# Kernel tuning notes

Hardware: AMD Instinct MI355X
Metric: run time of the kernel (lower is better)

The kernel has to match this reference:

```python
import jax, jax.numpy as jnp
import numpy as np

WS = 11
SIGMA = 1.5
CH = 3
C1 = (0.01 * 255.0) ** 2  # 6.5025
C2 = (0.03 * 255.0) ** 2  # 58.5225


def _gauss_window():
    # 1D Gaussian -> outer product -> depthwise kernel [C, 1, ws, ws] (OIHW)
    coords = jnp.arange(WS, dtype=jnp.float32) - WS // 2
    g = jnp.exp(-coords ** 2 / (2.0 * SIGMA ** 2))
    g = g / g.sum()
    w2d = g[:, None] * g[None, :]
    return jnp.tile(w2d[None, None], (CH, 1, 1, 1))


def _dwconv(x, win):
    pad = WS // 2
    return jax.lax.conv_general_dilated(
        x, win, window_strides=(1, 1), padding=[(pad, pad), (pad, pad)],
        feature_group_count=CH,
        dimension_numbers=('NCHW', 'OIHW', 'NCHW'))


def setup_inputs() -> dict:
    key = jax.random.key(0)
    k1, k2 = jax.random.split(key)
    shape = (32, 3, 512, 512)
    img_gen = jax.random.uniform(k1, shape, jnp.float32, -1.0, 1.0)
    img_ref = jax.random.uniform(k2, shape, jnp.float32, -1.0, 1.0)
    return {"img_gen": img_gen, "img_ref": img_ref}


def reference(img_gen, img_ref):
    gen = (img_gen + 1.0) * 0.5
    ref = (img_ref + 1.0) * 0.5
    win = _gauss_window()

    mu1 = _dwconv(gen, win)
    mu2 = _dwconv(ref, win)
    mu1_sq = mu1 * mu1
    mu2_sq = mu2 * mu2
    mu1_mu2 = mu1 * mu2
    sigma1_sq = _dwconv(gen * gen, win) - mu1_sq
    sigma2_sq = _dwconv(ref * ref, win) - mu2_sq
    sigma12 = _dwconv(gen * ref, win) - mu1_mu2

    ssim_map = ((2.0 * mu1_mu2 + C1) * (2.0 * sigma12 + C2)) / (
        (mu1_sq + mu2_sq + C1) * (sigma1_sq + sigma2_sq + C2))
    return 1.0 - ssim_map.mean()
```

## Files before the change

kernel.cpp:

```cpp
#include <hip/hip_runtime.h>

typedef float v2f __attribute__((ext_vector_type(2)));

#define TX 64
#define TY 8
#define MY 8
#define BYR (TY * MY)
#define WIN 26
#define HSTR 65
#define IMW 512
#define IMH 512
#define NPLANES 96
#define NBX (IMW / TX)
#define NBY (IMH / BYR)
#define NBLOCKS (NBX * NBY * NPLANES)

#define GW0 0.00102838f
#define GW1 0.00759877f
#define GW2 0.03600077f
#define GW3 0.10936069f
#define GW4 0.21300553f
#define GW5 0.26601172f

__device__ __forceinline__ void pkfma(v2f& acc, v2f a, v2f b) {
  asm("v_pk_fma_f32 %0, %1, %2, %0" : "+v"(acc) : "v"(a), "v"(b));
}
__device__ __forceinline__ v2f pkmul(v2f a, v2f b) {
  v2f d;
  asm("v_pk_mul_f32 %0, %1, %2" : "=v"(d) : "v"(a), "v"(b));
  return d;
}

__device__ __forceinline__ void hblur4(
    const float* __restrict__ gp, const float* __restrict__ rp,
    float* __restrict__ sq, int x0, bool fast, int nrows, int gy0,
    int slot0, int tid) {
  if (tid >= nrows * 16) return;
  const float GW[11] = {GW0, GW1, GW2, GW3, GW4, GW5,
                        GW4, GW3, GW2, GW1, GW0};
  const int r = tid >> 4;
  const int xs = (tid & 15) * 4;
  const int gy = gy0 + r;
  int slot = slot0 + r;
  if (slot >= WIN) slot -= WIN;
  const int xbase = x0 + xs - 8;
  const float* grow = gp + (size_t)gy * IMW;
  const float* rrow = rp + (size_t)gy * IMW;

  v2f P[14];
#define PUT1(idx, gc, rc)                                                    \
  do {                                                                       \
    if ((idx) >= 3 && (idx) <= 16)                                           \
      P[(idx) - 3] = (v2f){fmaf(0.5f, (gc), 0.5f), fmaf(0.5f, (rc), 0.5f)};  \
  } while (0)
  if (fast) {
#pragma unroll
    for (int k = 0; k < 5; ++k) {
      const float4 g4 = *(const float4*)(grow + xbase + 4 * k);
      const float4 r4 = *(const float4*)(rrow + xbase + 4 * k);
      PUT1(4 * k + 0, g4.x, r4.x);
      PUT1(4 * k + 1, g4.y, r4.y);
      PUT1(4 * k + 2, g4.z, r4.z);
      PUT1(4 * k + 3, g4.w, r4.w);
    }
  } else {
    const bool rowok = (gy >= 0) & (gy < IMH);
#pragma unroll
    for (int k = 0; k < 5; ++k) {
      const int c = xbase + 4 * k;
      const bool ok = rowok && (c >= 0) && (c < IMW);
      float4 g4 = make_float4(-1.f, -1.f, -1.f, -1.f);
      float4 r4 = g4;
      if (ok) {
        g4 = *(const float4*)(grow + c);
        r4 = *(const float4*)(rrow + c);
      }
      PUT1(4 * k + 0, g4.x, r4.x);
      PUT1(4 * k + 1, g4.y, r4.y);
      PUT1(4 * k + 2, g4.z, r4.z);
      PUT1(4 * k + 3, g4.w, r4.w);
    }
  }
#undef PUT1

  v2f accP[4], accQ[4];
  float accS[4];
#pragma unroll
  for (int o = 0; o < 4; ++o) {
    accP[o] = (v2f){0.f, 0.f};
    accQ[o] = (v2f){0.f, 0.f};
    accS[o] = 0.f;
  }

#pragma unroll
  for (int p = 0; p < 14; ++p) {
    const v2f pv = P[p];
    const v2f qv = pkmul(pv, pv);
    const float sv = pv.x * pv.y;
    const int olo = (p - 10 < 0) ? 0 : p - 10;
    const int ohi = (p < 3) ? p : 3;
#pragma unroll
    for (int o = olo; o <= ohi; ++o) {
      const float wt = GW[p - o];
      const v2f wv = (v2f){wt, wt};
      pkfma(accP[o], wv, pv);
      pkfma(accQ[o], wv, qv);
      accS[o] = fmaf(wt, sv, accS[o]);
    }
  }

  float* dst = sq + slot * (5 * HSTR) + xs;
#pragma unroll
  for (int o = 0; o < 4; ++o) dst[0 * HSTR + o] = accP[o].x;
#pragma unroll
  for (int o = 0; o < 4; ++o) dst[1 * HSTR + o] = accP[o].y;
#pragma unroll
  for (int o = 0; o < 4; ++o) dst[2 * HSTR + o] = accQ[o].x;
#pragma unroll
  for (int o = 0; o < 4; ++o) dst[3 * HSTR + o] = accQ[o].y;
#pragma unroll
  for (int o = 0; o < 4; ++o) dst[4 * HSTR + o] = accS[o];
}

__device__ __forceinline__ float ssim_px(v2f mu, v2f ee, float e12) {
  const float C1 = 6.5025f, C2 = 58.5225f;
  const float mu1 = mu.x, mu2 = mu.y, e1 = ee.x, e2 = ee.y;
  const float m12 = mu1 * mu2;
  const float m1s = mu1 * mu1;
  const float m2s = mu2 * mu2;
  const float num = (2.f * m12 + C1) * (2.f * (e12 - m12) + C2);
  const float den = (m1s + m2s + C1) * ((e1 - m1s) + (e2 - m2s) + C2);
  return __fdividef(num, den);
}

__device__ __forceinline__ float phase2(
    const float* __restrict__ sq, int wb, int col, int r0) {
  const float GW[11] = {GW0, GW1, GW2, GW3, GW4, GW5,
                        GW4, GW3, GW2, GW1, GW0};
  v2f mu[4], ee[4];
  float e12[4];
#pragma unroll
  for (int o = 0; o < 4; ++o) {
    mu[o] = (v2f){0.f, 0.f};
    ee[o] = (v2f){0.f, 0.f};
    e12[o] = 0.f;
  }
#pragma unroll
  for (int i = 0; i < 15; ++i) {
    int slot = wb + r0 + i;
    if (slot >= WIN) slot -= WIN;
    const float* rowp = sq + slot * (5 * HSTR) + col;
    const v2f hp = (v2f){rowp[0 * HSTR], rowp[1 * HSTR]};
    const v2f hq = (v2f){rowp[2 * HSTR], rowp[3 * HSTR]};
    const float hsv = rowp[4 * HSTR];
    const int olo = (i - 10 < 0) ? 0 : i - 10;
    const int ohi = (i < 3) ? i : 3;
#pragma unroll
    for (int o = olo; o <= ohi; ++o) {
      const float wt = GW[i - o];
      const v2f wv = (v2f){wt, wt};
      pkfma(mu[o], wv, hp);
      pkfma(ee[o], wv, hq);
      e12[o] = fmaf(wt, hsv, e12[o]);
    }
  }
  return (ssim_px(mu[0], ee[0], e12[0]) + ssim_px(mu[1], ee[1], e12[1])) +
         (ssim_px(mu[2], ee[2], e12[2]) + ssim_px(mu[3], ee[3], e12[3]));
}

__global__ __launch_bounds__(256, 4) void ssim_main(
    const float* __restrict__ gen, const float* __restrict__ ref,
    double* __restrict__ partial) {
  __shared__ float s_q[WIN][5][HSTR];
  float* const sq = &s_q[0][0][0];

  const int tid = threadIdx.x;
  const int bid = blockIdx.x;
  const int bx = bid & (NBX - 1);
  const int rem = bid >> 3;
  const int by = rem & (NBY - 1);
  const int plane = rem >> 3;
  const int x0 = bx * TX;
  const int Y0 = by * BYR;
  const float* gp = gen + (size_t)plane * (IMW * IMH);
  const float* rp = ref + (size_t)plane * (IMW * IMH);
  const bool ix = (bx >= 1) & (bx <= NBX - 2);

  const int col = tid & 63;
  const int r0 = __builtin_amdgcn_readfirstlane((tid >> 6 >= 3) ? 4 : 0);

  hblur4(gp, rp, sq, x0, ix & (by > 0), 16, Y0 - 5, 0, tid);
  hblur4(gp, rp, sq, x0, ix, 2, Y0 + 11, 16, tid);
  __syncthreads();

  double acc = 0.0;
  int wbase = 0;
  int sbase = 18;
#pragma unroll 1
  for (int c = 0; c < MY; ++c) {
    if (tid < 128) {
      if (c < MY - 1) {
        const int gy0 = Y0 + 13 + TY * c;
        hblur4(gp, rp, sq, x0, ix && (gy0 + TY <= IMH), TY, gy0, sbase, tid);
      }
    } else {
      acc += (double)phase2(sq, wbase, col, r0);
    }
    __syncthreads();
    wbase += TY;
    if (wbase >= WIN) wbase -= WIN;
    sbase += TY;
    if (sbase >= WIN) sbase -= WIN;
  }

#pragma unroll
  for (int off = 32; off > 0; off >>= 1) acc += __shfl_down(acc, off, 64);
  double* swsum = (double*)sq;
  if ((tid & 63) == 0) swsum[tid >> 6] = acc;
  __syncthreads();
  if (tid == 0) partial[bid] = swsum[0] + swsum[1] + swsum[2] + swsum[3];
}

__global__ void ssim_reduce(const double* __restrict__ partial,
                            float* __restrict__ out) {
  const int tid = threadIdx.x;
  double s = 0.0;
  for (int i = tid; i < NBLOCKS; i += 256) s += partial[i];
#pragma unroll
  for (int off = 32; off > 0; off >>= 1) s += __shfl_down(s, off, 64);
  __shared__ double sd[4];
  if ((tid & 63) == 0) sd[tid >> 6] = s;
  __syncthreads();
  if (tid == 0) {
    const double npix = (double)NPLANES * (double)IMW * (double)IMH;
    out[0] = (float)(1.0 - (sd[0] + sd[1] + sd[2] + sd[3]) / npix);
  }
}

extern "C" void kernel_launch(void* const* d_in, const int* in_sizes, int n_in,
                              void* d_out, int out_size, void* d_ws, size_t ws_size,
                              hipStream_t stream) {
  (void)in_sizes; (void)n_in; (void)out_size; (void)ws_size;
  const float* gen = (const float*)d_in[0];
  const float* ref = (const float*)d_in[1];
  double* partial = (double*)d_ws;
  ssim_main<<<NBLOCKS, 256, 0, stream>>>(gen, ref, partial);
  ssim_reduce<<<1, 256, 0, stream>>>(partial, (float*)d_out);
}
```

Measured before the change: 325.8 us.

## Make each wavefront own a 32-column strip with a private ring buffer, dropping block barriers

Restructures the SSIM kernel so each 64-lane wavefront processes its own 32-wide, 256-row strip. Each wave keeps a private 18-row shared-memory ring of horizontal blur results and alternates vertical-blur and horizontal-blur steps itself, so the per-chunk __syncthreads calls go away. Partial sums are written per wave, and the launch-bounds occupancy hint drops from 4 to 3 blocks. In exchange, the narrower strips recompute more horizontal halo columns per output, each wave runs a serial chain of 32 chunks, and the compute/load split between waves inside a block is lost.

```diff
diff --git a/kernel.cpp b/kernel.cpp
--- a/kernel.cpp
+++ b/kernel.cpp
@@ -2,18 +2,19 @@
 
 typedef float v2f __attribute__((ext_vector_type(2)));
 
-#define TX 64
 #define TY 8
-#define MY 8
-#define BYR (TY * MY)
-#define WIN 26
-#define HSTR 65
+#define WIN 18
+#define CST 33
+#define RST (5 * CST)
+#define SWV (WIN * RST)
 #define IMW 512
 #define IMH 512
 #define NPLANES 96
-#define NBX (IMW / TX)
-#define NBY (IMH / BYR)
-#define NBLOCKS (NBX * NBY * NPLANES)
+#define NSX 16
+#define NSEG 2
+#define NCH 32
+#define NWAVES (NSX * NSEG * NPLANES)
+#define NBLOCKS (NWAVES / 4)
 
 #define GW0 0.00102838f
 #define GW1 0.00759877f
@@ -31,17 +32,15 @@
   return d;
 }
 
-__device__ __forceinline__ void hblur4(
+__device__ __forceinline__ void hblur(
     const float* __restrict__ gp, const float* __restrict__ rp,
     float* __restrict__ sq, int x0, bool fast, int nrows, int gy0,
-    int slot0, int tid) {
-  if (tid >= nrows * 16) return;
+    int slot0, int hr, int xs) {
+  if (hr >= nrows) return;
   const float GW[11] = {GW0, GW1, GW2, GW3, GW4, GW5,
                         GW4, GW3, GW2, GW1, GW0};
-  const int r = tid >> 4;
-  const int xs = (tid & 15) * 4;
-  const int gy = gy0 + r;
-  int slot = slot0 + r;
+  const int gy = gy0 + hr;
+  int slot = slot0 + hr;
   if (slot >= WIN) slot -= WIN;
   const int xbase = x0 + xs - 8;
   const float* grow = gp + (size_t)gy * IMW;
@@ -109,17 +108,17 @@
     }
   }
 
-  float* dst = sq + slot * (5 * HSTR) + xs;
-#pragma unroll
-  for (int o = 0; o < 4; ++o) dst[0 * HSTR + o] = accP[o].x;
-#pragma unroll
-  for (int o = 0; o < 4; ++o) dst[1 * HSTR + o] = accP[o].y;
-#pragma unroll
-  for (int o = 0; o < 4; ++o) dst[2 * HSTR + o] = accQ[o].x;
-#pragma unroll
-  for (int o = 0; o < 4; ++o) dst[3 * HSTR + o] = accQ[o].y;
-#pragma unroll
-  for (int o = 0; o < 4; ++o) dst[4 * HSTR + o] = accS[o];
+  float* dst = sq + slot * RST + xs;
+#pragma unroll
+  for (int o = 0; o < 4; ++o) dst[0 * CST + o] = accP[o].x;
+#pragma unroll
+  for (int o = 0; o < 4; ++o) dst[1 * CST + o] = accP[o].y;
+#pragma unroll
+  for (int o = 0; o < 4; ++o) dst[2 * CST + o] = accQ[o].x;
+#pragma unroll
+  for (int o = 0; o < 4; ++o) dst[3 * CST + o] = accQ[o].y;
+#pragma unroll
+  for (int o = 0; o < 4; ++o) dst[4 * CST + o] = accS[o];
 }
 
 __device__ __forceinline__ float ssim_px(v2f mu, v2f ee, float e12) {
@@ -133,7 +132,7 @@
   return __fdividef(num, den);
 }
 
-__device__ __forceinline__ float phase2(
+__device__ __forceinline__ float vchunk(
     const float* __restrict__ sq, int wb, int col, int r0) {
   const float GW[11] = {GW0, GW1, GW2, GW3, GW4, GW5,
                         GW4, GW3, GW2, GW1, GW0};
@@ -146,13 +145,13 @@
     e12[o] = 0.f;
   }
 #pragma unroll
-  for (int i = 0; i < 15; ++i) {
+  for (int i = 0; i < 14; ++i) {
     int slot = wb + r0 + i;
     if (slot >= WIN) slot -= WIN;
-    const float* rowp = sq + slot * (5 * HSTR) + col;
-    const v2f hp = (v2f){rowp[0 * HSTR], rowp[1 * HSTR]};
-    const v2f hq = (v2f){rowp[2 * HSTR], rowp[3 * HSTR]};
-    const float hsv = rowp[4 * HSTR];
+    const float* rowp = sq + slot * RST + col;
+    const v2f hp = (v2f){rowp[0 * CST], rowp[1 * CST]};
+    const v2f hq = (v2f){rowp[2 * CST], rowp[3 * CST]};
+    const float hsv = rowp[4 * CST];
     const int olo = (i - 10 < 0) ? 0 : i - 10;
     const int ohi = (i < 3) ? i : 3;
 #pragma unroll
@@ -168,64 +167,58 @@
          (ssim_px(mu[2], ee[2], e12[2]) + ssim_px(mu[3], ee[3], e12[3]));
 }
 
-__global__ __launch_bounds__(256, 4) void ssim_main(
+__global__ __launch_bounds__(256, 3) void ssim_main(
     const float* __restrict__ gen, const float* __restrict__ ref,
     double* __restrict__ partial) {
-  __shared__ float s_q[WIN][5][HSTR];
-  float* const sq = &s_q[0][0][0];
+  __shared__ float ring[4][SWV];
 
   const int tid = threadIdx.x;
-  const int bid = blockIdx.x;
-  const int bx = bid & (NBX - 1);
-  const int rem = bid >> 3;
-  const int by = rem & (NBY - 1);
-  const int plane = rem >> 3;
-  const int x0 = bx * TX;
-  const int Y0 = by * BYR;
+  const int wv = tid >> 6;
+  const int lane = tid & 63;
+  const int wid = (blockIdx.x << 2) | wv;
+  const int plane = wid >> 5;
+  const int rem = wid & 31;
+  const int sx = rem & 15;
+  const int seg = rem >> 4;
+  const int x0 = sx * 32;
+  const int Y0 = seg * 256;
   const float* gp = gen + (size_t)plane * (IMW * IMH);
   const float* rp = ref + (size_t)plane * (IMW * IMH);
-  const bool ix = (bx >= 1) & (bx <= NBX - 2);
-
-  const int col = tid & 63;
-  const int r0 = __builtin_amdgcn_readfirstlane((tid >> 6 >= 3) ? 4 : 0);
-
-  hblur4(gp, rp, sq, x0, ix & (by > 0), 16, Y0 - 5, 0, tid);
-  hblur4(gp, rp, sq, x0, ix, 2, Y0 + 11, 16, tid);
-  __syncthreads();
+  float* const sq = &ring[wv][0];
+  const bool fx = (sx >= 1) & (sx <= NSX - 2);
+
+  const int hr = lane >> 3;
+  const int xs = (lane & 7) * 4;
+  const int col = lane & 31;
+  const int r0 = (lane >> 5) * 4;
+
+  hblur(gp, rp, sq, x0, fx & (seg > 0), 8, Y0 - 5, 0, hr, xs);
+  hblur(gp, rp, sq, x0, fx, 8, Y0 + 3, 8, hr, xs);
+  hblur(gp, rp, sq, x0, fx, 2, Y0 + 11, 16, hr, xs);
 
   double acc = 0.0;
-  int wbase = 0;
-  int sbase = 18;
+  int wb = 0;
 #pragma unroll 1
-  for (int c = 0; c < MY; ++c) {
-    if (tid < 128) {
-      if (c < MY - 1) {
-        const int gy0 = Y0 + 13 + TY * c;
-        hblur4(gp, rp, sq, x0, ix && (gy0 + TY <= IMH), TY, gy0, sbase, tid);
-      }
-    } else {
-      acc += (double)phase2(sq, wbase, col, r0);
-    }
-    __syncthreads();
-    wbase += TY;
-    if (wbase >= WIN) wbase -= WIN;
-    sbase += TY;
-    if (sbase >= WIN) sbase -= WIN;
+  for (int c = 0; c < NCH; ++c) {
+    acc += (double)vchunk(sq, wb, col, r0);
+    if (c < NCH - 1) {
+      const int gy0 = Y0 + 13 + TY * c;
+      hblur(gp, rp, sq, x0, fx && (gy0 + TY <= IMH), TY, gy0, wb, hr, xs);
+    }
+    wb += TY;
+    if (wb >= WIN) wb -= WIN;
   }
 
 #pragma unroll
   for (int off = 32; off > 0; off >>= 1) acc += __shfl_down(acc, off, 64);
-  double* swsum = (double*)sq;
-  if ((tid & 63) == 0) swsum[tid >> 6] = acc;
-  __syncthreads();
-  if (tid == 0) partial[bid] = swsum[0] + swsum[1] + swsum[2] + swsum[3];
+  if (lane == 0) partial[wid] = acc;
 }
 
 __global__ void ssim_reduce(const double* __restrict__ partial,
                             float* __restrict__ out) {
   const int tid = threadIdx.x;
   double s = 0.0;
-  for (int i = tid; i < NBLOCKS; i += 256) s += partial[i];
+  for (int i = tid; i < NWAVES; i += 256) s += partial[i];
 #pragma unroll
   for (int off = 32; off > 0; off >>= 1) s += __shfl_down(s, off, 64);
   __shared__ double sd[4];
```

Result: faster. 299.1 us (-8.2%).
